# Kernel optimization log

Hardware: AMD Instinct MI355X
Metric: run time of the kernel (lower is better)

Reference implementation:

```python
import jax, jax.numpy as jnp
import numpy as np

N = 50000          # number of input/output nodes (M == N since out_features=None)
E = 1_600_000      # total neighbor entries (avg degree 32)
C_IN = 64
HID = 128
C_OUT = 64


def setup_inputs() -> dict:
    key = jax.random.key(0)
    k1, k2, k3, k4, k5 = jax.random.split(key, 5)
    in_features = jax.random.normal(k1, (N, C_IN), dtype=jnp.float32)
    # MLP params: Linear(2C->HID), GELU, Linear(HID->C_OUT)
    W1 = jax.random.normal(k2, (2 * C_IN, HID), dtype=jnp.float32) * (1.0 / np.sqrt(2 * C_IN))
    b1 = jnp.zeros((HID,), dtype=jnp.float32)
    W2 = jax.random.normal(k3, (HID, C_OUT), dtype=jnp.float32) * (1.0 / np.sqrt(HID))
    b2 = jnp.zeros((C_OUT,), dtype=jnp.float32)
    neighbors_index = jax.random.randint(k4, (E,), 0, N, dtype=jnp.int64)
    # row_splits: sorted, starts at 0, ends at E (CSR-style ragged offsets)
    inner = jnp.sort(jax.random.randint(k5, (N - 1,), 0, E, dtype=jnp.int64))
    neighbors_row_splits = jnp.concatenate(
        [jnp.zeros((1,), jnp.int64), inner, jnp.full((1,), E, jnp.int64)])
    return {
        "in_features": in_features,
        "W1": W1, "b1": b1, "W2": W2, "b2": b2,
        "neighbors_index": neighbors_index,
        "neighbors_row_splits": neighbors_row_splits,
    }


def reference(in_features, W1, b1, W2, b2, neighbors_index, neighbors_row_splits):
    rs = neighbors_row_splits
    counts = rs[1:] - rs[:-1]                                  # [M] num_reps per row
    # segment id of each edge: row i owns edges [rs[i], rs[i+1])
    seg_ids = jnp.searchsorted(rs[1:], jnp.arange(E), side="right")  # [E]

    rep_features = in_features[neighbors_index]                # gather neighbors [E, C]
    self_features = in_features[seg_ids]                       # repeat_interleave  [E, C]
    agg = jnp.concatenate([rep_features, self_features], axis=1)  # [E, 2C]

    h = jax.nn.gelu(agg @ W1 + b1, approximate=False)          # torch GELU = exact erf
    msg = h @ W2 + b2                                          # [E, C_out]

    summed = jax.ops.segment_sum(msg, seg_ids, num_segments=N)  # [M, C_out]
    denom = jnp.maximum(counts, 1).astype(msg.dtype)[:, None]
    return summed / denom                                       # mean reduction
```

## Files before the change

### kernel.cpp

```cpp
#include <hip/hip_runtime.h>
#include <hip/hip_bf16.h>
#include <math.h>

#define C_IN  64
#define HID   128
#define C_OUT 64

typedef __attribute__((ext_vector_type(8))) short s16x8;
typedef __attribute__((ext_vector_type(4))) float f32x4;
typedef __attribute__((ext_vector_type(2))) float f32x2;

__device__ __forceinline__ f32x2 gelu2(f32x2 x) {
    f32x2 t  = x * x;
    f32x2 p  = t * 0.10294455f + 2.30211462f;
    f32x2 xp = x * p;
    f32x2 E;
    E.x = __builtin_amdgcn_exp2f(xp.x);
    E.y = __builtin_amdgcn_exp2f(xp.y);
    f32x2 Ep = E + 1.0f;
    f32x2 r;
    r.x = __builtin_amdgcn_rcpf(Ep.x);
    r.y = __builtin_amdgcn_rcpf(Ep.y);
    return x - x * r;
}

__device__ __forceinline__ float4 fma4(float s, float4 w, float4 acc) {
    acc.x = fmaf(s, w.x, acc.x); acc.y = fmaf(s, w.y, acc.y);
    acc.z = fmaf(s, w.z, acc.z); acc.w = fmaf(s, w.w, acc.w);
    return acc;
}

__device__ __forceinline__ unsigned pk_bf16(float lo, float hi) {
    union { __hip_bfloat162 v; unsigned u; } cv;
    cv.v = __float22bfloat162_rn(make_float2(lo, hi));
    return cv.u;
}
__device__ __forceinline__ f32x2 unpk2(unsigned p) {
    union { unsigned u; float f; } lo, hi;
    lo.u = p << 16; hi.u = p & 0xffff0000u;
    f32x2 v; v.x = lo.f; v.y = hi.f; return v;
}

#define K1_NODES 64

__global__ __launch_bounds__(512, 2) void precompute_ab(
    const float* __restrict__ X, const float* __restrict__ W1,
    const float* __restrict__ b1, const float* __restrict__ W2,
    const int* __restrict__ rs,
    unsigned* __restrict__ A16, float* __restrict__ B,
    unsigned short* __restrict__ W2T, int* __restrict__ bsplit,
    int N, int E, int G)
{
    __shared__ float W1s[2 * C_IN * HID];
    __shared__ float xs[K1_NODES * C_IN];
    int tid = threadIdx.x;

    for (int i = tid; i < (2 * C_IN * HID) / 4; i += 512)
        ((float4*)W1s)[i] = ((const float4*)W1)[i];

    int base = blockIdx.x * K1_NODES;
    int nLoc = min(K1_NODES, N - base);
    for (int i = tid; i < nLoc * (C_IN / 4); i += 512)
        ((float4*)xs)[i] = ((const float4*)(X + (size_t)base * C_IN))[i];

    if (blockIdx.x == 0) {
        for (int i = tid; i < C_OUT * HID; i += 512) {
            int c = i >> 7, k = i & (HID - 1);
            W2T[i] = (unsigned short)pk_bf16(W2[k * C_OUT + c], 0.f);
        }
    }

    {
        int gi = blockIdx.x * 512 + tid;
        if (gi <= G) {
            int t = (int)(((long long)E * gi) / G);
            int lo = 0, hi = N;
            while (lo < hi) { int mm = (lo + hi) >> 1; if (rs[mm] < t) lo = mm + 1; else hi = mm; }
            bsplit[gi] = lo;
        }
    }

    __syncthreads();

    int quad = (tid & 31) * 4;
    int slot = tid >> 5;
    int s0   = slot * 4;
    if (s0 >= nLoc) return;

    float4 a0 = {}, a1 = {}, a2 = {}, a3 = {};
    float4 b0 = {}, b1r = {}, b2r = {}, b3 = {};

    const float* xr0 = xs + (s0 + 0) * C_IN;
    const float* xr1 = xs + (s0 + 1) * C_IN;
    const float* xr2 = xs + (s0 + 2) * C_IN;
    const float* xr3 = xs + (s0 + 3) * C_IN;

#define K1STEP(c, CMP)                                                      \
    do {                                                                    \
        float4 wa = *(const float4*)&W1s[(c) * HID + quad];                 \
        float4 wb = *(const float4*)&W1s[((c) + C_IN) * HID + quad];        \
        a0 = fma4(xv0.CMP, wa, a0); b0  = fma4(xv0.CMP, wb, b0);            \
        a1 = fma4(xv1.CMP, wa, a1); b1r = fma4(xv1.CMP, wb, b1r);           \
        a2 = fma4(xv2.CMP, wa, a2); b2r = fma4(xv2.CMP, wb, b2r);           \
        a3 = fma4(xv3.CMP, wa, a3); b3  = fma4(xv3.CMP, wb, b3);            \
    } while (0)

#pragma unroll 1
    for (int c4 = 0; c4 < C_IN; c4 += 4) {
        float4 xv0 = *(const float4*)&xr0[c4];
        float4 xv1 = *(const float4*)&xr1[c4];
        float4 xv2 = *(const float4*)&xr2[c4];
        float4 xv3 = *(const float4*)&xr3[c4];
        K1STEP(c4 + 0, x);
        K1STEP(c4 + 1, y);
        K1STEP(c4 + 2, z);
        K1STEP(c4 + 3, w);
    }
#undef K1STEP

    float4 bb = *(const float4*)(b1 + quad);
    b0.x += bb.x;  b0.y += bb.y;  b0.z += bb.z;  b0.w += bb.w;
    b1r.x += bb.x; b1r.y += bb.y; b1r.z += bb.z; b1r.w += bb.w;
    b2r.x += bb.x; b2r.y += bb.y; b2r.z += bb.z; b2r.w += bb.w;
    b3.x += bb.x;  b3.y += bb.y;  b3.z += bb.z;  b3.w += bb.w;

    int adw = (base + s0) * (HID / 2) + (quad >> 1);
    size_t boff = (size_t)(base + s0) * HID + quad;
    if (s0 + 0 < nLoc) {
        uint2 u = { pk_bf16(a0.x, a0.y), pk_bf16(a0.z, a0.w) };
        *(uint2*)(A16 + adw) = u;              *(float4*)(B + boff) = b0;
    }
    if (s0 + 1 < nLoc) {
        uint2 u = { pk_bf16(a1.x, a1.y), pk_bf16(a1.z, a1.w) };
        *(uint2*)(A16 + adw + HID / 2) = u;    *(float4*)(B + boff + HID) = b1r;
    }
    if (s0 + 2 < nLoc) {
        uint2 u = { pk_bf16(a2.x, a2.y), pk_bf16(a2.z, a2.w) };
        *(uint2*)(A16 + adw + HID) = u;        *(float4*)(B + boff + 2 * HID) = b2r;
    }
    if (s0 + 3 < nLoc) {
        uint2 u = { pk_bf16(a3.x, a3.y), pk_bf16(a3.z, a3.w) };
        *(uint2*)(A16 + adw + 3 * (HID / 2)) = u; *(float4*)(B + boff + 3 * HID) = b3;
    }
}

#define EA_WAVES 4

#define EA_ISSUE(P0,P1,P2,P3, g) do { int _s8 = ((g) << 3) + half;            \
    int _i0 = __shfl(idx, _s8);                                               \
    int _i1 = __shfl(idx, _s8 + 2);                                           \
    int _i2 = __shfl(idx, _s8 + 4);                                           \
    int _i3 = __shfl(idx, _s8 + 6);                                           \
    P0 = *(const uint2*)(A8 + ((((unsigned)_i0) << 8) | lb));                 \
    P1 = *(const uint2*)(A8 + ((((unsigned)_i1) << 8) | lb));                 \
    P2 = *(const uint2*)(A8 + ((((unsigned)_i2) << 8) | lb));                 \
    P3 = *(const uint2*)(A8 + ((((unsigned)_i3) << 8) | lb));                 \
} while (0)

#define EA_PROC1(P) do {                                                      \
    acc01 += gelu2(unpk2(P.x) + bb01);                                        \
    acc23 += gelu2(unpk2(P.y) + bb23); } while (0)

#define EA_PROC1M(P, p) do {                                                  \
    float _mk = ((((p) << 1) + half) < m) ? 1.f : 0.f;                        \
    acc01 += gelu2(unpk2(P.x) + bb01) * _mk;                                  \
    acc23 += gelu2(unpk2(P.y) + bb23) * _mk; } while (0)

#define EA_PROCG(P0,P1,P2,P3, g) do {                                         \
    if ((((g) + 1) << 3) <= m) { EA_PROC1(P0); EA_PROC1(P1);                  \
                                 EA_PROC1(P2); EA_PROC1(P3); }                \
    else { int _p = (g) << 2;                                                 \
           EA_PROC1M(P0, _p);                                                 \
           if (((_p + 1) << 1) < m) EA_PROC1M(P1, _p + 1);                    \
           if (((_p + 2) << 1) < m) EA_PROC1M(P2, _p + 2);                    \
           if (((_p + 3) << 1) < m) EA_PROC1M(P3, _p + 3); } } while (0)

__global__ __launch_bounds__(256, 4) void edge_agg(
    const unsigned* __restrict__ A16, const float* __restrict__ B,
    const int* __restrict__ nbr, const int* __restrict__ rs,
    const int* __restrict__ bsplit,
    unsigned* __restrict__ Hout, int N, int E, int G)
{
    int wave = threadIdx.x >> 6, lane = threadIdx.x & 63;
    int half = lane >> 5, l5 = lane & 31;
    const char* A8 = (const char*)A16;
    unsigned lb = (unsigned)(l5 << 3);
    int b = blockIdx.x;

    int r0 = bsplit[b];
    int r1 = (b == G - 1) ? N : bsplit[b + 1];

    int row = r0 + wave;
    if (row >= r1) return;

    int s = rs[row], e = rs[row + 1];
    float4 bb4 = *(const float4*)(B + (size_t)row * HID + l5 * 4);
    int idx = 0;
    if (e > s) { int mn = min(64, e - s); idx = nbr[s + min(lane, mn - 1)]; }

    for (;;) {
        int cnt = e - s;

        int nrow = row + EA_WAVES;
        bool hasn = nrow < r1;
        int sn = s, en = e;
        float4 bbn = bb4;
        if (hasn) {
            sn = rs[nrow]; en = rs[nrow + 1];
            bbn = *(const float4*)(B + (size_t)nrow * HID + l5 * 4);
        }

        f32x2 bb01, bb23;
        bb01.x = bb4.x; bb01.y = bb4.y; bb23.x = bb4.z; bb23.y = bb4.w;
        f32x2 acc01 = {0.f, 0.f}, acc23 = {0.f, 0.f};

        if (cnt > 0) {
            int cs = s;
            for (;;) {
                int m = min(64, e - cs);
                int ng = (m + 7) >> 3;

                uint2 A0, A1, A2, A3, B0, B1, B2, B3, C0, C1, C2, C3;
                EA_ISSUE(A0, A1, A2, A3, 0);
                if (ng > 1) EA_ISSUE(B0, B1, B2, B3, 1);

                int ncs = cs + 64;
                int idx_next = idx;
                if (ncs < e) {
                    int mn = min(64, e - ncs);
                    idx_next = nbr[ncs + min(lane, mn - 1)];
                } else if (hasn && en > sn) {
                    int mn = min(64, en - sn);
                    idx_next = nbr[sn + min(lane, mn - 1)];
                }

                int g = 0;
                for (;;) {
                    if (g + 2 < ng) EA_ISSUE(C0, C1, C2, C3, g + 2);
                    EA_PROCG(A0, A1, A2, A3, g);
                    if (++g >= ng) break;
                    if (g + 2 < ng) EA_ISSUE(A0, A1, A2, A3, g + 2);
                    EA_PROCG(B0, B1, B2, B3, g);
                    if (++g >= ng) break;
                    if (g + 2 < ng) EA_ISSUE(B0, B1, B2, B3, g + 2);
                    EA_PROCG(C0, C1, C2, C3, g);
                    if (++g >= ng) break;
                }

                idx = idx_next;
                if (ncs >= e) break;
                cs = ncs;
            }
        } else if (hasn && en > sn) {
            int mn = min(64, en - sn);
            idx = nbr[sn + min(lane, mn - 1)];
        }

        acc01.x += __shfl_xor(acc01.x, 32);
        acc01.y += __shfl_xor(acc01.y, 32);
        acc23.x += __shfl_xor(acc23.x, 32);
        acc23.y += __shfl_xor(acc23.y, 32);

        if (half == 0) {
            float sc = (cnt > 0) ? 1.f / (float)cnt : 0.f;
            uint2 o = { pk_bf16(acc01.x * sc, acc01.y * sc),
                        pk_bf16(acc23.x * sc, acc23.y * sc) };
            ((uint2*)(Hout + (size_t)row * (HID / 2)))[l5] = o;
        }

        if (!hasn) break;
        row = nrow; s = sn; e = en; bb4 = bbn;
    }
}

#undef EA_ISSUE
#undef EA_PROC1
#undef EA_PROC1M
#undef EA_PROCG

__global__ __launch_bounds__(256) void h_w2_mfma(
    const unsigned short* __restrict__ H, const unsigned short* __restrict__ W2T,
    const float* __restrict__ b2, const int* __restrict__ rs,
    float* __restrict__ out, int N)
{
    int wave = threadIdx.x >> 6, lane = threadIdx.x & 63;
    int base = (blockIdx.x * 4 + wave) * 16;
    if (base >= N) return;

    int r16 = lane & 15;
    int kg  = lane >> 4;

    const unsigned short* hrow = H + (size_t)(base + r16) * HID + kg * 8;
    const unsigned short* wc0  = W2T + (size_t)(0 * 16 + r16) * HID + kg * 8;
    const unsigned short* wc1  = W2T + (size_t)(1 * 16 + r16) * HID + kg * 8;
    const unsigned short* wc2  = W2T + (size_t)(2 * 16 + r16) * HID + kg * 8;
    const unsigned short* wc3  = W2T + (size_t)(3 * 16 + r16) * HID + kg * 8;

    f32x4 acc0 = {0.f, 0.f, 0.f, 0.f};
    f32x4 acc1 = acc0, acc2 = acc0, acc3 = acc0;

#pragma unroll
    for (int kk = 0; kk < 4; ++kk) {
        s16x8 a  = *(const s16x8*)(hrow + kk * 32);
        s16x8 f0 = *(const s16x8*)(wc0 + kk * 32);
        s16x8 f1 = *(const s16x8*)(wc1 + kk * 32);
        s16x8 f2 = *(const s16x8*)(wc2 + kk * 32);
        s16x8 f3 = *(const s16x8*)(wc3 + kk * 32);
        acc0 = __builtin_amdgcn_mfma_f32_16x16x32_bf16(a, f0, acc0, 0, 0, 0);
        acc1 = __builtin_amdgcn_mfma_f32_16x16x32_bf16(a, f1, acc1, 0, 0, 0);
        acc2 = __builtin_amdgcn_mfma_f32_16x16x32_bf16(a, f2, acc2, 0, 0, 0);
        acc3 = __builtin_amdgcn_mfma_f32_16x16x32_bf16(a, f3, acc3, 0, 0, 0);
    }

    float bia0 = b2[r16], bia1 = b2[16 + r16], bia2 = b2[32 + r16], bia3 = b2[48 + r16];

#pragma unroll
    for (int r = 0; r < 4; ++r) {
        int rowi = base + kg * 4 + r;
        if (rowi < N) {
            float mmk = (rs[rowi + 1] > rs[rowi]) ? 1.f : 0.f;
            float* o = out + (size_t)rowi * C_OUT;
            o[r16]      = mmk * (acc0[r] + bia0);
            o[16 + r16] = mmk * (acc1[r] + bia1);
            o[32 + r16] = mmk * (acc2[r] + bia2);
            o[48 + r16] = mmk * (acc3[r] + bia3);
        }
    }
}

extern "C" void kernel_launch(void* const* d_in, const int* in_sizes, int n_in,
                              void* d_out, int out_size, void* d_ws, size_t ws_size,
                              hipStream_t stream) {
    const float* X  = (const float*)d_in[0];
    const float* W1 = (const float*)d_in[1];
    const float* b1 = (const float*)d_in[2];
    const float* W2 = (const float*)d_in[3];
    const float* b2 = (const float*)d_in[4];
    const int*   nbr = (const int*)d_in[5];
    const int*   rs  = (const int*)d_in[6];
    float* outp = (float*)d_out;

    int N = in_sizes[6] - 1;
    int E = in_sizes[5];

    int G = 3072;

    unsigned*       A16  = (unsigned*)d_ws;
    float*          Bbuf = (float*)(A16 + (size_t)N * (HID / 2));
    unsigned*       Hout = (unsigned*)(Bbuf + (size_t)N * HID);
    unsigned short* W2T  = (unsigned short*)(Hout + (size_t)N * (HID / 2));
    int*            bsplit = (int*)(W2T + C_OUT * HID);

    int g1 = (N + K1_NODES - 1) / K1_NODES;
    hipLaunchKernelGGL(precompute_ab, dim3(g1), dim3(512), 0, stream,
                       X, W1, b1, W2, rs, A16, Bbuf, W2T, bsplit, N, E, G);

    hipLaunchKernelGGL(edge_agg, dim3(G), dim3(256), 0, stream,
                       A16, Bbuf, nbr, rs, bsplit, Hout, N, E, G);

    int stripes = (N + 15) / 16;
    int g3 = (stripes + 3) / 4;
    hipLaunchKernelGGL(h_w2_mfma, dim3(g3), dim3(256), 0, stream,
                       (const unsigned short*)Hout, W2T, b2, rs, outp, N);
}
```

Baseline: 139.7 us.

## Fuse edge aggregation with W2 MFMA projection via shared-memory tiles

The edge aggregation and the second linear layer are merged into one kernel. Each block stages 16 aggregated bf16 hidden rows in LDS and immediately runs the MFMA projection plus bias and mask, so the hidden matrix no longer makes a round trip through global memory and one launch is removed. Blocks shrink to two waves and the grid grows so each block owns fewer rows, which keeps enough blocks for parallelism. The cost is per-tile barriers and MFMA work wasted on partially filled 16-row tiles, since most blocks hold only a few rows.

```diff
diff --git a/kernel.cpp b/kernel.cpp
--- a/kernel.cpp
+++ b/kernel.cpp
@@ -5,6 +5,7 @@
 #define C_IN  64
 #define HID   128
 #define C_OUT 64
+#define K1_NODES 64
 
 typedef __attribute__((ext_vector_type(8))) short s16x8;
 typedef __attribute__((ext_vector_type(4))) float f32x4;
@@ -41,8 +42,6 @@
     f32x2 v; v.x = lo.f; v.y = hi.f; return v;
 }
 
-#define K1_NODES 64
-
 __global__ __launch_bounds__(512, 2) void precompute_ab(
     const float* __restrict__ X, const float* __restrict__ W1,
     const float* __restrict__ b1, const float* __restrict__ W2,
@@ -144,7 +143,8 @@
     }
 }
 
-#define EA_WAVES 4
+#define EA_WAVES 2
+#define HS_STR 136
 
 #define EA_ISSUE(P0,P1,P2,P3, g) do { int _s8 = ((g) << 3) + half;            \
     int _i0 = __shfl(idx, _s8);                                               \
@@ -175,14 +175,18 @@
            if (((_p + 2) << 1) < m) EA_PROC1M(P2, _p + 2);                    \
            if (((_p + 3) << 1) < m) EA_PROC1M(P3, _p + 3); } } while (0)
 
-__global__ __launch_bounds__(256, 4) void edge_agg(
+__global__ __launch_bounds__(128) void edge_agg_fused(
     const unsigned* __restrict__ A16, const float* __restrict__ B,
     const int* __restrict__ nbr, const int* __restrict__ rs,
-    const int* __restrict__ bsplit,
-    unsigned* __restrict__ Hout, int N, int E, int G)
+    const int* __restrict__ bsplit, const unsigned short* __restrict__ W2T,
+    const float* __restrict__ b2, float* __restrict__ out,
+    int N, int E, int G)
 {
+    __shared__ unsigned short Hs[16 * HS_STR];
+
     int wave = threadIdx.x >> 6, lane = threadIdx.x & 63;
     int half = lane >> 5, l5 = lane & 31;
+    int r16 = lane & 15, kg = lane >> 4;
     const char* A8 = (const char*)A16;
     unsigned lb = (unsigned)(l5 << 3);
     int b = blockIdx.x;
@@ -190,86 +194,123 @@
     int r0 = bsplit[b];
     int r1 = (b == G - 1) ? N : bsplit[b + 1];
 
-    int row = r0 + wave;
-    if (row >= r1) return;
-
-    int s = rs[row], e = rs[row + 1];
-    float4 bb4 = *(const float4*)(B + (size_t)row * HID + l5 * 4);
-    int idx = 0;
-    if (e > s) { int mn = min(64, e - s); idx = nbr[s + min(lane, mn - 1)]; }
-
-    for (;;) {
-        int cnt = e - s;
-
-        int nrow = row + EA_WAVES;
-        bool hasn = nrow < r1;
-        int sn = s, en = e;
-        float4 bbn = bb4;
-        if (hasn) {
-            sn = rs[nrow]; en = rs[nrow + 1];
-            bbn = *(const float4*)(B + (size_t)nrow * HID + l5 * 4);
-        }
-
-        f32x2 bb01, bb23;
-        bb01.x = bb4.x; bb01.y = bb4.y; bb23.x = bb4.z; bb23.y = bb4.w;
-        f32x2 acc01 = {0.f, 0.f}, acc23 = {0.f, 0.f};
-
-        if (cnt > 0) {
-            int cs = s;
+    for (int tb = r0; tb < r1; tb += 16) {
+        int te = min(tb + 16, r1);
+
+        int row = tb + wave;
+        if (row < te) {
+            int s = rs[row], e = rs[row + 1];
+            float4 bb4 = *(const float4*)(B + (size_t)row * HID + l5 * 4);
+            int idx = 0;
+            if (e > s) { int mn = min(64, e - s); idx = nbr[s + min(lane, mn - 1)]; }
+
             for (;;) {
-                int m = min(64, e - cs);
-                int ng = (m + 7) >> 3;
-
-                uint2 A0, A1, A2, A3, B0, B1, B2, B3, C0, C1, C2, C3;
-                EA_ISSUE(A0, A1, A2, A3, 0);
-                if (ng > 1) EA_ISSUE(B0, B1, B2, B3, 1);
-
-                int ncs = cs + 64;
-                int idx_next = idx;
-                if (ncs < e) {
-                    int mn = min(64, e - ncs);
-                    idx_next = nbr[ncs + min(lane, mn - 1)];
+                int cnt = e - s;
+
+                int nrow = row + EA_WAVES;
+                bool hasn = nrow < te;
+                int sn = s, en = e;
+                float4 bbn = bb4;
+                if (hasn) {
+                    sn = rs[nrow]; en = rs[nrow + 1];
+                    bbn = *(const float4*)(B + (size_t)nrow * HID + l5 * 4);
+                }
+
+                f32x2 bb01, bb23;
+                bb01.x = bb4.x; bb01.y = bb4.y; bb23.x = bb4.z; bb23.y = bb4.w;
+                f32x2 acc01 = {0.f, 0.f}, acc23 = {0.f, 0.f};
+
+                if (cnt > 0) {
+                    int cs = s;
+                    for (;;) {
+                        int m = min(64, e - cs);
+                        int ng = (m + 7) >> 3;
+
+                        uint2 A0, A1, A2, A3, B0, B1, B2, B3, C0, C1, C2, C3;
+                        EA_ISSUE(A0, A1, A2, A3, 0);
+                        if (ng > 1) EA_ISSUE(B0, B1, B2, B3, 1);
+
+                        int ncs = cs + 64;
+                        int idx_next = idx;
+                        if (ncs < e) {
+                            int mn = min(64, e - ncs);
+                            idx_next = nbr[ncs + min(lane, mn - 1)];
+                        } else if (hasn && en > sn) {
+                            int mn = min(64, en - sn);
+                            idx_next = nbr[sn + min(lane, mn - 1)];
+                        }
+
+                        int g = 0;
+                        for (;;) {
+                            if (g + 2 < ng) EA_ISSUE(C0, C1, C2, C3, g + 2);
+                            EA_PROCG(A0, A1, A2, A3, g);
+                            if (++g >= ng) break;
+                            if (g + 2 < ng) EA_ISSUE(A0, A1, A2, A3, g + 2);
+                            EA_PROCG(B0, B1, B2, B3, g);
+                            if (++g >= ng) break;
+                            if (g + 2 < ng) EA_ISSUE(B0, B1, B2, B3, g + 2);
+                            EA_PROCG(C0, C1, C2, C3, g);
+                            if (++g >= ng) break;
+                        }
+
+                        idx = idx_next;
+                        if (ncs >= e) break;
+                        cs = ncs;
+                    }
                 } else if (hasn && en > sn) {
                     int mn = min(64, en - sn);
-                    idx_next = nbr[sn + min(lane, mn - 1)];
+                    idx = nbr[sn + min(lane, mn - 1)];
                 }
 
-                int g = 0;
-                for (;;) {
-                    if (g + 2 < ng) EA_ISSUE(C0, C1, C2, C3, g + 2);
-                    EA_PROCG(A0, A1, A2, A3, g);
-                    if (++g >= ng) break;
-                    if (g + 2 < ng) EA_ISSUE(A0, A1, A2, A3, g + 2);
-                    EA_PROCG(B0, B1, B2, B3, g);
-                    if (++g >= ng) break;
-                    if (g + 2 < ng) EA_ISSUE(B0, B1, B2, B3, g + 2);
-                    EA_PROCG(C0, C1, C2, C3, g);
-                    if (++g >= ng) break;
+                acc01.x += __shfl_xor(acc01.x, 32);
+                acc01.y += __shfl_xor(acc01.y, 32);
+                acc23.x += __shfl_xor(acc23.x, 32);
+                acc23.y += __shfl_xor(acc23.y, 32);
+
+                if (half == 0) {
+                    float sc = (cnt > 0) ? 1.f / (float)cnt : 0.f;
+                    uint2 o = { pk_bf16(acc01.x * sc, acc01.y * sc),
+                                pk_bf16(acc23.x * sc, acc23.y * sc) };
+                    *(uint2*)(&Hs[(row - tb) * HS_STR + l5 * 4]) = o;
                 }
 
-                idx = idx_next;
-                if (ncs >= e) break;
-                cs = ncs;
+                if (!hasn) break;
+                row = nrow; s = sn; e = en; bb4 = bbn;
             }
-        } else if (hasn && en > sn) {
-            int mn = min(64, en - sn);
-            idx = nbr[sn + min(lane, mn - 1)];
         }
-
-        acc01.x += __shfl_xor(acc01.x, 32);
-        acc01.y += __shfl_xor(acc01.y, 32);
-        acc23.x += __shfl_xor(acc23.x, 32);
-        acc23.y += __shfl_xor(acc23.y, 32);
-
-        if (half == 0) {
-            float sc = (cnt > 0) ? 1.f / (float)cnt : 0.f;
-            uint2 o = { pk_bf16(acc01.x * sc, acc01.y * sc),
-                        pk_bf16(acc23.x * sc, acc23.y * sc) };
-            ((uint2*)(Hout + (size_t)row * (HID / 2)))[l5] = o;
+        __syncthreads();
+
+        {
+            const unsigned short* hrow = Hs + r16 * HS_STR + kg * 8;
+            int c0 = wave * 32;
+            const unsigned short* wcA = W2T + (size_t)(c0 + r16) * HID + kg * 8;
+            const unsigned short* wcB = W2T + (size_t)(c0 + 16 + r16) * HID + kg * 8;
+
+            f32x4 accA = {0.f, 0.f, 0.f, 0.f};
+            f32x4 accB = accA;
+#pragma unroll
+            for (int kk = 0; kk < 4; ++kk) {
+                s16x8 a  = *(const s16x8*)(hrow + kk * 32);
+                s16x8 fA = *(const s16x8*)(wcA + kk * 32);
+                s16x8 fB = *(const s16x8*)(wcB + kk * 32);
+                accA = __builtin_amdgcn_mfma_f32_16x16x32_bf16(a, fA, accA, 0, 0, 0);
+                accB = __builtin_amdgcn_mfma_f32_16x16x32_bf16(a, fB, accB, 0, 0, 0);
+            }
+
+            float biaA = b2[c0 + r16];
+            float biaB = b2[c0 + 16 + r16];
+#pragma unroll
+            for (int r = 0; r < 4; ++r) {
+                int rowi = tb + kg * 4 + r;
+                if (rowi < te) {
+                    float mmk = (rs[rowi + 1] > rs[rowi]) ? 1.f : 0.f;
+                    float* o = out + (size_t)rowi * C_OUT;
+                    o[c0 + r16]      = mmk * (accA[r] + biaA);
+                    o[c0 + 16 + r16] = mmk * (accB[r] + biaB);
+                }
+            }
         }
-
-        if (!hasn) break;
-        row = nrow; s = sn; e = en; bb4 = bbn;
+        __syncthreads();
     }
 }
 
@@ -277,56 +318,6 @@
 #undef EA_PROC1
 #undef EA_PROC1M
 #undef EA_PROCG
-
-__global__ __launch_bounds__(256) void h_w2_mfma(
-    const unsigned short* __restrict__ H, const unsigned short* __restrict__ W2T,
-    const float* __restrict__ b2, const int* __restrict__ rs,
-    float* __restrict__ out, int N)
-{
-    int wave = threadIdx.x >> 6, lane = threadIdx.x & 63;
-    int base = (blockIdx.x * 4 + wave) * 16;
-    if (base >= N) return;
-
-    int r16 = lane & 15;
-    int kg  = lane >> 4;
-
-    const unsigned short* hrow = H + (size_t)(base + r16) * HID + kg * 8;
-    const unsigned short* wc0  = W2T + (size_t)(0 * 16 + r16) * HID + kg * 8;
-    const unsigned short* wc1  = W2T + (size_t)(1 * 16 + r16) * HID + kg * 8;
-    const unsigned short* wc2  = W2T + (size_t)(2 * 16 + r16) * HID + kg * 8;
-    const unsigned short* wc3  = W2T + (size_t)(3 * 16 + r16) * HID + kg * 8;
-
-    f32x4 acc0 = {0.f, 0.f, 0.f, 0.f};
-    f32x4 acc1 = acc0, acc2 = acc0, acc3 = acc0;
-
-#pragma unroll
-    for (int kk = 0; kk < 4; ++kk) {
-        s16x8 a  = *(const s16x8*)(hrow + kk * 32);
-        s16x8 f0 = *(const s16x8*)(wc0 + kk * 32);
-        s16x8 f1 = *(const s16x8*)(wc1 + kk * 32);
-        s16x8 f2 = *(const s16x8*)(wc2 + kk * 32);
-        s16x8 f3 = *(const s16x8*)(wc3 + kk * 32);
-        acc0 = __builtin_amdgcn_mfma_f32_16x16x32_bf16(a, f0, acc0, 0, 0, 0);
-        acc1 = __builtin_amdgcn_mfma_f32_16x16x32_bf16(a, f1, acc1, 0, 0, 0);
-        acc2 = __builtin_amdgcn_mfma_f32_16x16x32_bf16(a, f2, acc2, 0, 0, 0);
-        acc3 = __builtin_amdgcn_mfma_f32_16x16x32_bf16(a, f3, acc3, 0, 0, 0);
-    }
-
-    float bia0 = b2[r16], bia1 = b2[16 + r16], bia2 = b2[32 + r16], bia3 = b2[48 + r16];
-
-#pragma unroll
-    for (int r = 0; r < 4; ++r) {
-        int rowi = base + kg * 4 + r;
-        if (rowi < N) {
-            float mmk = (rs[rowi + 1] > rs[rowi]) ? 1.f : 0.f;
-            float* o = out + (size_t)rowi * C_OUT;
-            o[r16]      = mmk * (acc0[r] + bia0);
-            o[16 + r16] = mmk * (acc1[r] + bia1);
-            o[32 + r16] = mmk * (acc2[r] + bia2);
-            o[48 + r16] = mmk * (acc3[r] + bia3);
-        }
-    }
-}
 
 extern "C" void kernel_launch(void* const* d_in, const int* in_sizes, int n_in,
                               void* d_out, int out_size, void* d_ws, size_t ws_size,
@@ -343,23 +334,17 @@
     int N = in_sizes[6] - 1;
     int E = in_sizes[5];
 
-    int G = 3072;
+    int G = 12288;
 
     unsigned*       A16  = (unsigned*)d_ws;
     float*          Bbuf = (float*)(A16 + (size_t)N * (HID / 2));
-    unsigned*       Hout = (unsigned*)(Bbuf + (size_t)N * HID);
-    unsigned short* W2T  = (unsigned short*)(Hout + (size_t)N * (HID / 2));
+    unsigned short* W2T  = (unsigned short*)(Bbuf + (size_t)N * HID);
     int*            bsplit = (int*)(W2T + C_OUT * HID);
 
     int g1 = (N + K1_NODES - 1) / K1_NODES;
     hipLaunchKernelGGL(precompute_ab, dim3(g1), dim3(512), 0, stream,
                        X, W1, b1, W2, rs, A16, Bbuf, W2T, bsplit, N, E, G);
 
-    hipLaunchKernelGGL(edge_agg, dim3(G), dim3(256), 0, stream,
-                       A16, Bbuf, nbr, rs, bsplit, Hout, N, E, G);
-
-    int stripes = (N + 15) / 16;
-    int g3 = (stripes + 3) / 4;
-    hipLaunchKernelGGL(h_w2_mfma, dim3(g3), dim3(256), 0, stream,
-                       (const unsigned short*)Hout, W2T, b2, rs, outp, N);
-}
+    hipLaunchKernelGGL(edge_agg_fused, dim3(G), dim3(128), 0, stream,
+                       A16, Bbuf, nbr, rs, bsplit, W2T, b2, outp, N, E, G);
+}
```

Measured after the change: 158.8 us. 1.14x slower.
